# Kernel tuning notes

Measured on AMD Instinct MI355X. Metric: run time of the kernel, lower is better.

## Reference

```python
import jax, jax.numpy as jnp
import numpy as np

DIM = 512
HEADS = 8
DIM_HEAD = 64
CROSS_DIM = 768
FF_INNER = 4 * DIM  # 2048
SCALE = DIM_HEAD ** -0.5
EPS = 1e-5


def _layer_norm(x, g, b):
    mu = jnp.mean(x, axis=-1, keepdims=True)
    var = jnp.var(x, axis=-1, keepdims=True)
    return (x - mu) * jax.lax.rsqrt(var + EPS) * g + b


def _mha(q, k, v):
    # q: [B,Sq,D], k/v: [B,Sk,D] -> [B,Sq,D]
    B, Sq, D = q.shape
    Sk = k.shape[1]
    qh = q.reshape(B, Sq, HEADS, DIM_HEAD).transpose(0, 2, 1, 3)
    kh = k.reshape(B, Sk, HEADS, DIM_HEAD).transpose(0, 2, 1, 3)
    vh = v.reshape(B, Sk, HEADS, DIM_HEAD).transpose(0, 2, 1, 3)
    scores = jnp.einsum('bhqd,bhkd->bhqk', qh, kh) * SCALE
    probs = jax.nn.softmax(scores, axis=-1)
    out = jnp.einsum('bhqk,bhkd->bhqd', probs, vh)
    return out.transpose(0, 2, 1, 3).reshape(B, Sq, D)


def setup_inputs() -> dict:
    key = jax.random.key(0)
    ks = jax.random.split(key, 20)
    s = 0.02
    inp = {
        'x': jax.random.normal(ks[0], (8, 1024, DIM), jnp.float32),
        'enc': jax.random.normal(ks[1], (8, 77, CROSS_DIM), jnp.float32),
        # self-attention (attn1)
        'ln1_g': jnp.ones((DIM,), jnp.float32),
        'ln1_b': jnp.zeros((DIM,), jnp.float32),
        'wq1': jax.random.normal(ks[2], (DIM, DIM), jnp.float32) * s,
        'wk1': jax.random.normal(ks[3], (DIM, DIM), jnp.float32) * s,
        'wv1': jax.random.normal(ks[4], (DIM, DIM), jnp.float32) * s,
        'wo1': jax.random.normal(ks[5], (DIM, DIM), jnp.float32) * s,
        'bo1': jnp.zeros((DIM,), jnp.float32),
        # cross-attention (attn2)
        'ln2_g': jnp.ones((DIM,), jnp.float32),
        'ln2_b': jnp.zeros((DIM,), jnp.float32),
        'wq2': jax.random.normal(ks[6], (DIM, DIM), jnp.float32) * s,
        'wk2': jax.random.normal(ks[7], (CROSS_DIM, DIM), jnp.float32) * s,
        'wv2': jax.random.normal(ks[8], (CROSS_DIM, DIM), jnp.float32) * s,
        'wo2': jax.random.normal(ks[9], (DIM, DIM), jnp.float32) * s,
        'bo2': jnp.zeros((DIM,), jnp.float32),
        # feed-forward (GEGLU)
        'ln3_g': jnp.ones((DIM,), jnp.float32),
        'ln3_b': jnp.zeros((DIM,), jnp.float32),
        'wg': jax.random.normal(ks[10], (DIM, 2 * FF_INNER), jnp.float32) * s,
        'bg': jnp.zeros((2 * FF_INNER,), jnp.float32),
        'wf': jax.random.normal(ks[11], (FF_INNER, DIM), jnp.float32) * s,
        'bf': jnp.zeros((DIM,), jnp.float32),
    }
    return inp


def reference(x, enc, ln1_g, ln1_b, wq1, wk1, wv1, wo1, bo1,
              ln2_g, ln2_b, wq2, wk2, wv2, wo2, bo2,
              ln3_g, ln3_b, wg, bg, wf, bf):
    # self-attention block (pre-norm)
    h = _layer_norm(x, ln1_g, ln1_b)
    a = _mha(h @ wq1, h @ wk1, h @ wv1)
    x = x + a @ wo1 + bo1
    # cross-attention block (pre-norm)
    h = _layer_norm(x, ln2_g, ln2_b)
    a = _mha(h @ wq2, enc @ wk2, enc @ wv2)
    x = x + a @ wo2 + bo2
    # GEGLU feed-forward (pre-norm)
    h = _layer_norm(x, ln3_g, ln3_b)
    proj = h @ wg + bg
    u, g = jnp.split(proj, 2, axis=-1)
    ff = (u * jax.nn.gelu(g, approximate=False)) @ wf + bf
    return x + ff
```

## Files before the change

kernel.cpp:

```cpp
#include <hip/hip_runtime.h>


typedef _Float16 half8 __attribute__((ext_vector_type(8)));
typedef float f32x4 __attribute__((ext_vector_type(4)));

__device__ __forceinline__ f32x4 mfma16(half8 a, half8 b, f32x4 c) {
  return __builtin_amdgcn_mfma_f32_16x16x32_f16(a, b, c, 0, 0, 0);
}

__device__ __forceinline__ void gload16(const _Float16* g, _Float16* l) {
  __builtin_amdgcn_global_load_lds(
      (const __attribute__((address_space(1))) void*)g,
      (__attribute__((address_space(3))) void*)l, 16, 0, 0);
}

__global__ __launch_bounds__(256)
void transpose_cvt(const float* __restrict__ src, _Float16* __restrict__ dst,
                   int K, int N) {
  __shared__ float tile[32][33];
  const int tx = threadIdx.x, ty = threadIdx.y;
  const int n0 = blockIdx.x * 32, k0 = blockIdx.y * 32;
  #pragma unroll
  for (int j = ty; j < 32; j += 8)
    tile[j][tx] = src[(size_t)(k0 + j) * N + n0 + tx];
  __syncthreads();
  #pragma unroll
  for (int j = ty; j < 32; j += 8)
    dst[(size_t)(n0 + j) * K + k0 + tx] = (_Float16)tile[tx][j];
}

__global__ void cvt_f32_f16(const float* __restrict__ src,
                            _Float16* __restrict__ dst, int n) {
  int i = blockIdx.x * 256 + threadIdx.x;
  if (i < n) dst[i] = (_Float16)src[i];
}

__global__ __launch_bounds__(256)
void vt_kernel(const _Float16* __restrict__ src, _Float16* __restrict__ dst,
               int S, int srcStride, int dstStride) {
  __shared__ _Float16 tile[32][33];
  const int tx = threadIdx.x, ty = threadIdx.y;
  const int s0 = blockIdx.x * 32, d0 = blockIdx.y * 32, bh = blockIdx.z;
  const int b = bh >> 3, h = bh & 7;
  const _Float16* sp = src + (size_t)b * S * srcStride + h * 64 + d0;
  #pragma unroll
  for (int j = ty; j < 32; j += 8) {
    int s = s0 + j; if (s >= S) s = S - 1;
    tile[j][tx] = sp[(size_t)s * srcStride + tx];
  }
  __syncthreads();
  _Float16* dp = dst + ((size_t)bh * 64 + d0) * dstStride + s0;
  #pragma unroll
  for (int j = ty; j < 32; j += 8)
    dp[(size_t)j * dstStride + tx] = tile[tx][j];
}

__global__ __launch_bounds__(256)
void ln_kernel(const float* __restrict__ x, const float* __restrict__ g,
               const float* __restrict__ b, _Float16* __restrict__ out) {
  const int row = blockIdx.x, t = threadIdx.x;
  const float* xr = x + (size_t)row * 512;
  float v0 = xr[t], v1 = xr[t + 256];
  float s1 = v0 + v1, s2 = v0 * v0 + v1 * v1;
  #pragma unroll
  for (int m = 32; m >= 1; m >>= 1) {
    s1 += __shfl_xor(s1, m);
    s2 += __shfl_xor(s2, m);
  }
  __shared__ float red[8];
  if ((t & 63) == 0) { red[t >> 6] = s1; red[4 + (t >> 6)] = s2; }
  __syncthreads();
  s1 = red[0] + red[1] + red[2] + red[3];
  s2 = red[4] + red[5] + red[6] + red[7];
  const float mu = s1 * (1.0f / 512.0f);
  const float var = s2 * (1.0f / 512.0f) - mu * mu;
  const float rs = rsqrtf(var + 1e-5f);
  out[(size_t)row * 512 + t] = (_Float16)((v0 - mu) * rs * g[t] + b[t]);
  out[(size_t)row * 512 + t + 256] =
      (_Float16)((v1 - mu) * rs * g[t + 256] + b[t + 256]);
}

template <int EPI, int GWM, int GWN, int WM, int WN, int MW>
__global__ __launch_bounds__(256, MW)
void gemm_bt(const _Float16* __restrict__ A, const _Float16* __restrict__ BT,
             int M, int N, int K, int lda, int ldc,
             _Float16* Ch, float* Cf,
             const float* __restrict__ bias, const float* resid) {
  constexpr int BM = GWM * WM * 16;
  constexpr int BN = GWN * WN * 16;
  __shared__ __align__(16) _Float16 As[4 * BM * 8];
  __shared__ __align__(16) _Float16 Bs[4 * BN * 8];
  __shared__ __align__(16) _Float16 Bs2[(EPI == 2) ? 4 * BN * 8 : 8];

  const int t = threadIdx.x;
  const int m0 = blockIdx.y * BM, n0 = blockIdx.x * BN;
  const int lane = t & 63, wv = t >> 6;
  const int quad = lane >> 4, l15 = lane & 15;
  const int wm = wv / GWN, wn = wv % GWN;

  f32x4 zero4 = {0.f, 0.f, 0.f, 0.f};
  f32x4 acc[WM][WN];
  f32x4 acc2[(EPI == 2) ? WM : 1][(EPI == 2) ? WN : 1];
  #pragma unroll
  for (int mi = 0; mi < WM; mi++)
    #pragma unroll
    for (int ni = 0; ni < WN; ni++) acc[mi][ni] = zero4;
  if constexpr (EPI == 2) {
    #pragma unroll
    for (int mi = 0; mi < WM; mi++)
      #pragma unroll
      for (int ni = 0; ni < WN; ni++) acc2[mi][ni] = zero4;
  }

  for (int k0 = 0; k0 < K; k0 += 32) {
    #pragma unroll
    for (int c = wv; c < BM / 16; c += 4) {
      const int s = c * 64 + lane;
      const int q = s / BM;
      int r = s % BM;
      int rg = m0 + r; if (rg >= M) rg = M - 1;
      gload16(A + (size_t)rg * lda + k0 + q * 8, As + c * 512);
    }
    #pragma unroll
    for (int c = wv; c < BN / 16; c += 4) {
      const int s = c * 64 + lane;
      const int q = s / BN;
      const int r = s % BN;
      gload16(BT + (size_t)(n0 + r) * K + k0 + q * 8, Bs + c * 512);
      if constexpr (EPI == 2)
        gload16(BT + (size_t)(2048 + n0 + r) * K + k0 + q * 8, Bs2 + c * 512);
    }
    __syncthreads();

    half8 fa[WM], fb[WN], fb2[(EPI == 2) ? WN : 1];
    #pragma unroll
    for (int mi = 0; mi < WM; mi++)
      fa[mi] = *(const half8*)(As +
          ((size_t)quad * BM + wm * WM * 16 + mi * 16 + l15) * 8);
    #pragma unroll
    for (int ni = 0; ni < WN; ni++) {
      fb[ni] = *(const half8*)(Bs +
          ((size_t)quad * BN + wn * WN * 16 + ni * 16 + l15) * 8);
      if constexpr (EPI == 2)
        fb2[ni] = *(const half8*)(Bs2 +
            ((size_t)quad * BN + wn * WN * 16 + ni * 16 + l15) * 8);
    }
    #pragma unroll
    for (int mi = 0; mi < WM; mi++)
      #pragma unroll
      for (int ni = 0; ni < WN; ni++) {
        acc[mi][ni] = mfma16(fa[mi], fb[ni], acc[mi][ni]);
        if constexpr (EPI == 2)
          acc2[mi][ni] = mfma16(fa[mi], fb2[ni], acc2[mi][ni]);
      }
    __syncthreads();
  }

  #pragma unroll
  for (int mi = 0; mi < WM; mi++) {
    const int rbase = m0 + wm * WM * 16 + mi * 16 + quad * 4;
    #pragma unroll
    for (int r = 0; r < 4; r++) {
      const int row = rbase + r;
      if (row >= M) continue;
      #pragma unroll
      for (int ni = 0; ni < WN; ni++) {
        const int col = n0 + wn * WN * 16 + ni * 16 + l15;
        const float v = acc[mi][ni][r];
        if constexpr (EPI == 0) {
          Ch[(size_t)row * ldc + col] = (_Float16)v;
        } else if constexpr (EPI == 1) {
          Cf[(size_t)row * ldc + col] =
              resid[(size_t)row * ldc + col] + v + bias[col];
        } else {
          const float u = v + bias[col];
          const float gg = acc2[mi][ni][r] + bias[col + 2048];
          const float ge = 0.5f * gg * (1.0f + erff(gg * 0.70710678118f));
          Ch[(size_t)row * ldc + col] = (_Float16)(u * ge);
        }
      }
    }
  }
}

__global__ __launch_bounds__(256)
void attn2(const _Float16* __restrict__ Q, const _Float16* __restrict__ K,
           const _Float16* __restrict__ VT, _Float16* __restrict__ O,
           int qStride, int kStride, long kBatchStride,
           int vtStride, int Sk) {
  __shared__ __align__(16) _Float16 KsL[2048];
  __shared__ __align__(16) _Float16 VTsL[2048];
  __shared__ __align__(16) _Float16 Ps[4][2][16][40];

  const int t = threadIdx.x;
  const int w = t >> 6, lane = t & 63, quad = lane >> 4, l15 = lane & 15;
  const int bh = blockIdx.y, b = bh >> 3, h = bh & 7;
  const int q0 = blockIdx.x * 128 + w * 32;

  const _Float16 qscale = (_Float16)(0.125f * 1.44269504f);
  half8 qf[2][2];
  #pragma unroll
  for (int mi = 0; mi < 2; mi++)
    #pragma unroll
    for (int c = 0; c < 2; c++) {
      const _Float16* qp = Q +
          (size_t)(b * 1024 + q0 + mi * 16 + l15) * qStride +
          h * 64 + c * 32 + quad * 8;
      half8 v = *(const half8*)qp;
      #pragma unroll
      for (int j = 0; j < 8; j++) v[j] *= qscale;
      qf[mi][c] = v;
    }

  f32x4 zero4 = {0.f, 0.f, 0.f, 0.f};
  f32x4 oa[2][4];
  float psum[2][4];
  #pragma unroll
  for (int mi = 0; mi < 2; mi++) {
    #pragma unroll
    for (int nt = 0; nt < 4; nt++) oa[mi][nt] = zero4;
    #pragma unroll
    for (int r = 0; r < 4; r++) psum[mi][r] = 0.f;
  }

  const _Float16* kp = K + (size_t)b * kBatchStride + h * 64;
  const _Float16* vtp = VT + (size_t)bh * 64 * vtStride;
  const int ksk = t & 31, kc = t >> 7, kqd = (t >> 5) & 3;
  const int vd = t & 63, vqd = t >> 6;

  for (int skb = 0; skb < Sk; skb += 32) {
    int skc = skb + ksk; if (skc >= Sk) skc = Sk - 1;
    gload16(kp + (size_t)skc * kStride + kc * 32 + kqd * 8, KsL + t * 8);
    gload16(vtp + (size_t)vd * vtStride + skb + vqd * 8, VTsL + t * 8);
    __syncthreads();

    const bool tail = (skb + 32 > Sk);
    #pragma unroll
    for (int mi = 0; mi < 2; mi++) {
      #pragma unroll
      for (int ct = 0; ct < 2; ct++) {
        f32x4 s = zero4;
        half8 kb0 = *(const half8*)(KsL + (quad * 32 + ct * 16 + l15) * 8);
        half8 kb1 = *(const half8*)(KsL + (128 + quad * 32 + ct * 16 + l15) * 8);
        s = mfma16(qf[mi][0], kb0, s);
        s = mfma16(qf[mi][1], kb1, s);
        if (tail) {
          const bool valid = (skb + ct * 16 + l15) < Sk;
          #pragma unroll
          for (int r = 0; r < 4; r++)
            if (!valid) s[r] = -__builtin_inff();
        }
        #pragma unroll
        for (int r = 0; r < 4; r++) {
          const float e = exp2f(s[r]);
          psum[mi][r] += e;
          Ps[w][mi][quad * 4 + r][ct * 16 + l15] = (_Float16)e;
        }
      }
    }
    #pragma unroll
    for (int mi = 0; mi < 2; mi++) {
      const half8 pf = *(const half8*)(&Ps[w][mi][l15][quad * 8]);
      #pragma unroll
      for (int nt = 0; nt < 4; nt++) {
        const half8 vf = *(const half8*)(VTsL + (quad * 64 + nt * 16 + l15) * 8);
        oa[mi][nt] = mfma16(pf, vf, oa[mi][nt]);
      }
    }
    __syncthreads();
  }

  #pragma unroll
  for (int mi = 0; mi < 2; mi++)
    #pragma unroll
    for (int r = 0; r < 4; r++) {
      #pragma unroll
      for (int mm = 1; mm < 16; mm <<= 1)
        psum[mi][r] += __shfl_xor(psum[mi][r], mm);
      psum[mi][r] = 1.0f / psum[mi][r];
    }

  #pragma unroll
  for (int mi = 0; mi < 2; mi++)
    #pragma unroll
    for (int nt = 0; nt < 4; nt++)
      #pragma unroll
      for (int r = 0; r < 4; r++) {
        const size_t row = (size_t)(b * 1024 + q0 + mi * 16 + quad * 4 + r);
        O[row * 512 + h * 64 + nt * 16 + l15] =
            (_Float16)(oa[mi][nt][r] * psum[mi][r]);
      }
}

extern "C" void kernel_launch(void* const* d_in, const int* in_sizes, int n_in,
                              void* d_out, int out_size, void* d_ws,
                              size_t ws_size, hipStream_t stream) {
  const float* x    = (const float*)d_in[0];
  const float* enc  = (const float*)d_in[1];
  const float* ln1g = (const float*)d_in[2];
  const float* ln1b = (const float*)d_in[3];
  const float* wq1  = (const float*)d_in[4];
  const float* wk1  = (const float*)d_in[5];
  const float* wv1  = (const float*)d_in[6];
  const float* wo1  = (const float*)d_in[7];
  const float* bo1  = (const float*)d_in[8];
  const float* ln2g = (const float*)d_in[9];
  const float* ln2b = (const float*)d_in[10];
  const float* wq2  = (const float*)d_in[11];
  const float* wk2  = (const float*)d_in[12];
  const float* wv2  = (const float*)d_in[13];
  const float* wo2  = (const float*)d_in[14];
  const float* bo2  = (const float*)d_in[15];
  const float* ln3g = (const float*)d_in[16];
  const float* ln3b = (const float*)d_in[17];
  const float* wg   = (const float*)d_in[18];
  const float* bg   = (const float*)d_in[19];
  const float* wf   = (const float*)d_in[20];
  const float* bfp  = (const float*)d_in[21];
  float* out = (float*)d_out;

  char* ws = (char*)d_ws;
  _Float16* qkvT  = (_Float16*)(ws + 0);
  _Float16* q2T   = (_Float16*)(ws + 1572864);
  _Float16* kv2T  = (_Float16*)(ws + 2097152);
  _Float16* wo1T  = (_Float16*)(ws + 3670016);
  _Float16* wo2T  = (_Float16*)(ws + 4194304);
  _Float16* wgT   = (_Float16*)(ws + 4718592);
  _Float16* wfT   = (_Float16*)(ws + 8912896);
  _Float16* hbuf  = (_Float16*)(ws + 11010048);
  _Float16* qkv   = (_Float16*)(ws + 19398656);
  _Float16* q2b   = (_Float16*)(ws + 44564480);
  _Float16* kv2b  = (_Float16*)(ws + 52953088);
  _Float16* attnb = (_Float16*)(ws + 54214656);
  _Float16* ench  = (_Float16*)(ws + 62603264);
  _Float16* ffb   = (_Float16*)(ws + 19398656);
  _Float16* VTself = hbuf;
  _Float16* VTc    = ench;

  const dim3 tb(32, 8);
  transpose_cvt<<<dim3(16, 16), tb, 0, stream>>>(wq1, qkvT, 512, 512);
  transpose_cvt<<<dim3(16, 16), tb, 0, stream>>>(wk1, qkvT + 512 * 512, 512, 512);
  transpose_cvt<<<dim3(16, 16), tb, 0, stream>>>(wv1, qkvT + 1024 * 512, 512, 512);
  transpose_cvt<<<dim3(16, 16), tb, 0, stream>>>(wo1, wo1T, 512, 512);
  transpose_cvt<<<dim3(16, 16), tb, 0, stream>>>(wq2, q2T, 512, 512);
  transpose_cvt<<<dim3(16, 24), tb, 0, stream>>>(wk2, kv2T, 768, 512);
  transpose_cvt<<<dim3(16, 24), tb, 0, stream>>>(wv2, kv2T + 512 * 768, 768, 512);
  transpose_cvt<<<dim3(16, 16), tb, 0, stream>>>(wo2, wo2T, 512, 512);
  transpose_cvt<<<dim3(128, 16), tb, 0, stream>>>(wg, wgT, 512, 4096);
  transpose_cvt<<<dim3(16, 64), tb, 0, stream>>>(wf, wfT, 2048, 512);
  cvt_f32_f16<<<(473088 + 255) / 256, 256, 0, stream>>>(enc, ench, 473088);

  ln_kernel<<<8192, 256, 0, stream>>>(x, ln1g, ln1b, hbuf);
  gemm_bt<0, 2, 2, 4, 4, 2><<<dim3(12, 64), 256, 0, stream>>>(
      hbuf, qkvT, 8192, 1536, 512, 512, 1536, qkv, nullptr, nullptr, nullptr);
  vt_kernel<<<dim3(32, 2, 64), tb, 0, stream>>>(qkv + 1024, VTself, 1024, 1536, 1024);
  attn2<<<dim3(8, 64), 256, 0, stream>>>(qkv, qkv + 512, VTself, attnb,
                                         1536, 1536, (long)1024 * 1536,
                                         1024, 1024);
  gemm_bt<1, 1, 4, 4, 2, 3><<<dim3(4, 128), 256, 0, stream>>>(
      attnb, wo1T, 8192, 512, 512, 512, 512, nullptr, out, bo1, x);

  ln_kernel<<<8192, 256, 0, stream>>>(out, ln2g, ln2b, hbuf);
  gemm_bt<0, 1, 4, 4, 2, 3><<<dim3(4, 128), 256, 0, stream>>>(
      hbuf, q2T, 8192, 512, 512, 512, 512, q2b, nullptr, nullptr, nullptr);
  gemm_bt<0, 1, 4, 4, 2, 3><<<dim3(8, 10), 256, 0, stream>>>(
      ench, kv2T, 616, 1024, 768, 768, 1024, kv2b, nullptr, nullptr, nullptr);
  vt_kernel<<<dim3(3, 2, 64), tb, 0, stream>>>(kv2b + 512, VTc, 77, 1024, 96);
  attn2<<<dim3(8, 64), 256, 0, stream>>>(q2b, kv2b, VTc, attnb,
                                         512, 1024, (long)77 * 1024, 96, 77);
  gemm_bt<1, 1, 4, 4, 2, 3><<<dim3(4, 128), 256, 0, stream>>>(
      attnb, wo2T, 8192, 512, 512, 512, 512, nullptr, out, bo2, out);

  ln_kernel<<<8192, 256, 0, stream>>>(out, ln3g, ln3b, hbuf);
  gemm_bt<2, 2, 2, 4, 2, 2><<<dim3(32, 64), 256, 0, stream>>>(
      hbuf, wgT, 8192, 2048, 512, 512, 2048, ffb, nullptr, bg, nullptr);
  gemm_bt<1, 1, 4, 4, 2, 3><<<dim3(4, 128), 256, 0, stream>>>(
      ffb, wfT, 8192, 512, 2048, 2048, 512, nullptr, out, bfp, out);
}
```

Baseline: 496.1 us.

## Double-buffer LDS tiles in GEMM and attention to prefetch next K-step

Shared-memory staging buffers in both the GEMM and the attention kernel are doubled, and the next tile's global-to-LDS loads are issued before computing on the current tile. This removes the pre-compute barrier per iteration, so global load latency can overlap MFMA work. LDS usage doubles, which may reduce occupancy, and the correctness of the async LDS loads depends on the single trailing barrier ordering buffer reuse.

```diff
diff --git a/kernel.cpp b/kernel.cpp
--- a/kernel.cpp
+++ b/kernel.cpp
@@ -88,9 +88,10 @@
              const float* __restrict__ bias, const float* resid) {
   constexpr int BM = GWM * WM * 16;
   constexpr int BN = GWN * WN * 16;
-  __shared__ __align__(16) _Float16 As[4 * BM * 8];
-  __shared__ __align__(16) _Float16 Bs[4 * BN * 8];
-  __shared__ __align__(16) _Float16 Bs2[(EPI == 2) ? 4 * BN * 8 : 8];
+  __shared__ __align__(16) _Float16 As[2][4 * BM * 8];
+  __shared__ __align__(16) _Float16 Bs[2][4 * BN * 8];
+  __shared__ __align__(16) _Float16 Bs2[(EPI == 2) ? 2 : 1]
+                                      [(EPI == 2) ? 4 * BN * 8 : 8];
 
   const int t = threadIdx.x;
   const int m0 = blockIdx.y * BM, n0 = blockIdx.x * BN;
@@ -112,38 +113,47 @@
       for (int ni = 0; ni < WN; ni++) acc2[mi][ni] = zero4;
   }
 
-  for (int k0 = 0; k0 < K; k0 += 32) {
+  auto stageAll = [&](int k0, int pb) {
     #pragma unroll
     for (int c = wv; c < BM / 16; c += 4) {
       const int s = c * 64 + lane;
       const int q = s / BM;
-      int r = s % BM;
+      const int r = s % BM;
       int rg = m0 + r; if (rg >= M) rg = M - 1;
-      gload16(A + (size_t)rg * lda + k0 + q * 8, As + c * 512);
+      gload16(A + (size_t)rg * lda + k0 + q * 8, &As[pb][c * 512]);
     }
     #pragma unroll
     for (int c = wv; c < BN / 16; c += 4) {
       const int s = c * 64 + lane;
       const int q = s / BN;
       const int r = s % BN;
-      gload16(BT + (size_t)(n0 + r) * K + k0 + q * 8, Bs + c * 512);
+      gload16(BT + (size_t)(n0 + r) * K + k0 + q * 8, &Bs[pb][c * 512]);
       if constexpr (EPI == 2)
-        gload16(BT + (size_t)(2048 + n0 + r) * K + k0 + q * 8, Bs2 + c * 512);
-    }
-    __syncthreads();
+        gload16(BT + (size_t)(2048 + n0 + r) * K + k0 + q * 8,
+                &Bs2[pb][c * 512]);
+    }
+  };
+
+  stageAll(0, 0);
+  __syncthreads();
+
+  const int NIT = K >> 5;
+  for (int it = 0; it < NIT; ++it) {
+    const int cur = it & 1;
+    if (it + 1 < NIT) stageAll((it + 1) << 5, cur ^ 1);
 
     half8 fa[WM], fb[WN], fb2[(EPI == 2) ? WN : 1];
     #pragma unroll
     for (int mi = 0; mi < WM; mi++)
-      fa[mi] = *(const half8*)(As +
-          ((size_t)quad * BM + wm * WM * 16 + mi * 16 + l15) * 8);
+      fa[mi] = *(const half8*)(&As[cur]
+          [((size_t)quad * BM + wm * WM * 16 + mi * 16 + l15) * 8]);
     #pragma unroll
     for (int ni = 0; ni < WN; ni++) {
-      fb[ni] = *(const half8*)(Bs +
-          ((size_t)quad * BN + wn * WN * 16 + ni * 16 + l15) * 8);
+      fb[ni] = *(const half8*)(&Bs[cur]
+          [((size_t)quad * BN + wn * WN * 16 + ni * 16 + l15) * 8]);
       if constexpr (EPI == 2)
-        fb2[ni] = *(const half8*)(Bs2 +
-            ((size_t)quad * BN + wn * WN * 16 + ni * 16 + l15) * 8);
+        fb2[ni] = *(const half8*)(&Bs2[cur]
+            [((size_t)quad * BN + wn * WN * 16 + ni * 16 + l15) * 8]);
     }
     #pragma unroll
     for (int mi = 0; mi < WM; mi++)
@@ -188,8 +198,8 @@
            const _Float16* __restrict__ VT, _Float16* __restrict__ O,
            int qStride, int kStride, long kBatchStride,
            int vtStride, int Sk) {
-  __shared__ __align__(16) _Float16 KsL[2048];
-  __shared__ __align__(16) _Float16 VTsL[2048];
+  __shared__ __align__(16) _Float16 KsL[2][2048];
+  __shared__ __align__(16) _Float16 VTsL[2][2048];
   __shared__ __align__(16) _Float16 Ps[4][2][16][40];
 
   const int t = threadIdx.x;
@@ -228,11 +238,19 @@
   const int ksk = t & 31, kc = t >> 7, kqd = (t >> 5) & 3;
   const int vd = t & 63, vqd = t >> 6;
 
-  for (int skb = 0; skb < Sk; skb += 32) {
+  auto stageKV = [&](int skb, int pb) {
     int skc = skb + ksk; if (skc >= Sk) skc = Sk - 1;
-    gload16(kp + (size_t)skc * kStride + kc * 32 + kqd * 8, KsL + t * 8);
-    gload16(vtp + (size_t)vd * vtStride + skb + vqd * 8, VTsL + t * 8);
-    __syncthreads();
+    gload16(kp + (size_t)skc * kStride + kc * 32 + kqd * 8, &KsL[pb][t * 8]);
+    gload16(vtp + (size_t)vd * vtStride + skb + vqd * 8, &VTsL[pb][t * 8]);
+  };
+
+  stageKV(0, 0);
+  __syncthreads();
+
+  int it = 0;
+  for (int skb = 0; skb < Sk; skb += 32, ++it) {
+    const int cur = it & 1;
+    if (skb + 32 < Sk) stageKV(skb + 32, cur ^ 1);
 
     const bool tail = (skb + 32 > Sk);
     #pragma unroll
@@ -240,8 +258,9 @@
       #pragma unroll
       for (int ct = 0; ct < 2; ct++) {
         f32x4 s = zero4;
-        half8 kb0 = *(const half8*)(KsL + (quad * 32 + ct * 16 + l15) * 8);
-        half8 kb1 = *(const half8*)(KsL + (128 + quad * 32 + ct * 16 + l15) * 8);
+        half8 kb0 = *(const half8*)(&KsL[cur][(quad * 32 + ct * 16 + l15) * 8]);
+        half8 kb1 =
+            *(const half8*)(&KsL[cur][(128 + quad * 32 + ct * 16 + l15) * 8]);
         s = mfma16(qf[mi][0], kb0, s);
         s = mfma16(qf[mi][1], kb1, s);
         if (tail) {
@@ -263,7 +282,8 @@
       const half8 pf = *(const half8*)(&Ps[w][mi][l15][quad * 8]);
       #pragma unroll
       for (int nt = 0; nt < 4; nt++) {
-        const half8 vf = *(const half8*)(VTsL + (quad * 64 + nt * 16 + l15) * 8);
+        const half8 vf =
+            *(const half8*)(&VTsL[cur][(quad * 64 + nt * 16 + l15) * 8]);
         oa[mi][nt] = mfma16(pf, vf, oa[mi][nt]);
       }
     }
```

Measured after the change: 495.0 us. About the same (-0.2%).
